# Optimization experiments

Hardware: AMD Instinct MI355X
Metric: run time of the kernel (lower is better)

## Reference

```python
import jax, jax.numpy as jnp
import numpy as np

TGT_LEN, BS, SRC_LEN, VOCAB, DIM, EMB = 24, 16, 400, 32000, 256, 256


def setup_inputs() -> dict:
    key = jax.random.key(0)
    ks = jax.random.split(key, 16)
    g = lambda k, s, sc: jax.random.normal(k, s, dtype=jnp.float32) * sc
    return {
        "inputs": jax.random.randint(ks[0], (TGT_LEN, BS), 0, VOCAB),
        "src": jax.random.randint(ks[1], (SRC_LEN, BS), 0, VOCAB),
        "h_e": g(ks[2], (SRC_LEN, BS, DIM), 0.1),
        "h0": g(ks[3], (BS, DIM), 0.1),
        "c0": g(ks[4], (BS, DIM), 0.1),
        "W_emb": g(ks[5], (VOCAB, EMB), 0.05),
        "W_ih": g(ks[6], (4 * DIM, EMB), 0.05),
        "b_ih": g(ks[7], (4 * DIM,), 0.05),
        "W_hh": g(ks[8], (4 * DIM, DIM), 0.05),
        "b_hh": g(ks[9], (4 * DIM,), 0.05),
        "W_attn_enc": g(ks[10], (DIM, DIM), 0.05),
        "W_attn_dec": g(ks[11], (DIM, DIM), 0.05),
        "W_proj": g(ks[12], (EMB, 3 * DIM), 0.05),
        "W_u": g(ks[13], (1, 3 * DIM), 0.05),
        "b_u": g(ks[14], (1,), 0.05),
        "b_out": g(ks[15], (VOCAB, 1), 0.05),
        "pad_id": 1,
    }


def reference(inputs, src, h_e, h0, c0, W_emb, W_ih, b_ih, W_hh, b_hh,
              W_attn_enc, W_attn_dec, W_proj, W_u, b_u, b_out, pad_id):
    tgt_len, bs = inputs.shape
    vocab = W_emb.shape[0]
    dim = h0.shape[1]

    emb_seq = W_emb[inputs]                       # [T, bs, emb]
    # weight-shared output projection (sect 2.4), loop-invariant -> hoisted
    W_out = jnp.tanh(W_emb @ W_proj)              # [vocab, 3*dim]
    b_out_v = b_out[:, 0]                         # [vocab]
    w_u = W_u[0]                                  # [3*dim]
    src_ids = src.T                               # [bs, src_len]
    rows = jnp.arange(bs)[:, None]
    pos = jnp.arange(tgt_len)

    def lstm_cell(x, h, c):
        gates = x @ W_ih.T + b_ih + h @ W_hh.T + b_hh
        i, f, g_, o = jnp.split(gates, 4, axis=1)
        c_new = jax.nn.sigmoid(f) * c + jax.nn.sigmoid(i) * jnp.tanh(g_)
        h_new = jax.nn.sigmoid(o) * jnp.tanh(c_new)
        return h_new, c_new

    def step(carry, xs):
        h, c, E_hist, hd_hist = carry
        emb_t, t = xs
        h, c = lstm_cell(emb_t, h, c)
        hd_t = h                                   # [bs, dim]
        # --- temporal encoder intra-attention (eq. 3-5) ---
        q = hd_t @ W_attn_enc                      # [bs, dim]
        expE = jnp.exp(jnp.einsum('bd,sbd->bs', q, h_e))  # [bs, src]
        EE = jnp.where(t == 0, expE, expE / E_hist)
        E_hist = jnp.where(t == 0, expE, E_hist + expE)
        A_e = EE / EE.sum(axis=1, keepdims=True)
        c_e = jnp.einsum('bs,sbd->bd', A_e, h_e)
        # --- decoder intra-attention over hd_history (includes current step) ---
        hd_hist = hd_hist.at[t].set(hd_t)          # [T, bs, dim]
        qd = hd_t @ W_attn_dec
        Ed = jnp.einsum('bd,tbd->bt', qd, hd_hist)
        mask = pos[None, :] <= t
        EEd = jnp.where(mask, jnp.exp(Ed), 0.0)
        A_d = EEd / EEd.sum(axis=1, keepdims=True)
        cd = jnp.einsum('bt,tbd->bd', A_d, hd_hist)
        cd_t = jnp.where(t == 0, jnp.zeros_like(cd), cd)  # t==0: cd is zeros
        # --- pointer-generator (sect 2.3) ---
        feat = jnp.concatenate([hd_t, c_e, cd_t], axis=1)   # [bs, 3*dim]
        p_switch = jax.nn.sigmoid(feat @ w_u + b_u[0])       # [bs]
        logits = feat @ W_out.T + b_out_v                     # [bs, vocab]
        logits = logits.at[:, pad_id].set(-jnp.inf)
        p_gen = jax.nn.softmax(logits, axis=1)
        copy = jnp.zeros((bs, vocab), logits.dtype).at[rows, src_ids].add(A_e)
        scores_t = (copy + p_gen) * p_switch[:, None]
        return (h, c, E_hist, hd_hist), scores_t

    hd_hist0 = jnp.zeros((tgt_len, bs, dim), h0.dtype)
    E_hist0 = jnp.ones((bs, h_e.shape[0]), h0.dtype)
    _, scores = jax.lax.scan(step, (h0, c0, E_hist0, hd_hist0), (emb_seq, pos))
    return scores  # [T, bs, vocab] mixed copy/gen distribution per step
```

## Files before the change

### kernel.cpp

```cpp
#include <hip/hip_runtime.h>
#include <cstdint>
#include <cstddef>

#define TGT   24
#define BS    16
#define SRC   400
#define VOCABN 32000
#define DIM   256
#define NROW  (TGT*BS)
#define LSTM_NBLK 4

typedef __bf16 bf16_t;
typedef __bf16 v8bf __attribute__((ext_vector_type(8)));
typedef float  v4f  __attribute__((ext_vector_type(4)));
typedef unsigned int u32;

__device__ __forceinline__ float fast_tanh(float x) {
    float e = __expf(2.f*x);
    return 1.f - 2.f/(e + 1.f);
}

__global__ void k_prep(const float* __restrict__ Whh, const float* __restrict__ Wad,
                       const float* __restrict__ he,  const float* __restrict__ Wemb,
                       const float* __restrict__ Wproj, const float* __restrict__ Wae,
                       const float* __restrict__ Wih, const int* __restrict__ inputs,
                       const float* __restrict__ h0,
                       bf16_t* o_whh, bf16_t* o_wadT, bf16_t* o_he, bf16_t* o_heT,
                       bf16_t* o_wae, bf16_t* o_wih, bf16_t* o_wprojT, bf16_t* o_embA,
                       bf16_t* o_hhi, bf16_t* o_hlo)
{
    const long S0=262144, S1=65536, S2=1638400, S3=1638400, S4=65536, S5=262144, S6=196608, S7=98304, S8=4096;
    const long total = S0+S1+S2+S3+S4+S5+S6+S7+S8;
    for (long i = (long)blockIdx.x*blockDim.x + threadIdx.x; i < total;
         i += (long)gridDim.x*blockDim.x) {
        long j = i;
        if (j < S0) { o_whh[j] = (bf16_t)Whh[j]; continue; }           j -= S0;
        if (j < S1) { long n = j>>8, k = j&255; o_wadT[j] = (bf16_t)Wad[k*DIM + n]; continue; } j -= S1;
        if (j < S2) { o_he[j] = (bf16_t)he[j]; continue; }             j -= S2;
        if (j < S3) {
            long b = j / 102400, rem = j % 102400, d = rem / 400, s = rem % 400;
            o_heT[j] = (bf16_t)he[(s*BS + b)*DIM + d]; continue; }     j -= S3;
        if (j < S4) { o_wae[j] = (bf16_t)Wae[j]; continue; }           j -= S4;
        if (j < S5) { o_wih[j] = (bf16_t)Wih[j]; continue; }           j -= S5;
        if (j < S6) { long n = j>>8, k = j&255; o_wprojT[j] = (bf16_t)Wproj[k*768 + n]; continue; } j -= S6;
        if (j < S7) { long r = j>>8, k = j&255; o_embA[j] = (bf16_t)Wemb[(long)inputs[r]*DIM + k]; continue; } j -= S7;
        {
          float v = h0[j];
          bf16_t hi = (bf16_t)v;
          o_hhi[j] = hi; o_hlo[j] = (bf16_t)(v - (float)hi); }
    }
}

__device__ __forceinline__ void gemm_tile(
    const int tid, bf16_t* As, bf16_t* Bs,
    const bf16_t* __restrict__ A, const float* __restrict__ A32,
    const bf16_t* __restrict__ B,
    const int tileIdx, const int N, const int K, const int Ntiles, const int mode,
    float* __restrict__ outF, bf16_t* __restrict__ outB,
    const float* __restrict__ bias0, const float* __restrict__ bias1)
{
    const int mt   = tileIdx / Ntiles, nt = tileIdx % Ntiles;
    const int m0   = mt*128, n0 = nt*128;
    const int lane = tid & 63, wave = tid >> 6;
    const int wm   = wave >> 1, wn = wave & 1;
    const int quad = lane >> 4, l16 = lane & 15;

    v4f acc[4][4];
#pragma unroll
    for (int i=0;i<4;i++)
#pragma unroll
        for (int j=0;j<4;j++) acc[i][j] = (v4f){0.f,0.f,0.f,0.f};

    const int srow = tid >> 1, shalf = tid & 1;
    const bf16_t* Ag   = A   ? A   + (size_t)(m0+srow)*K + shalf*16 : nullptr;
    const float*  Ag32 = A32 ? A32 + (size_t)(m0+srow)*K + shalf*16 : nullptr;
    const bf16_t* Bg = B + (size_t)(n0+srow)*K + shalf*16;
    bf16_t* AsW = &As[srow*40 + shalf*16];
    bf16_t* BsW = &Bs[srow*40 + shalf*16];

    for (int kc = 0; kc < K; kc += 32) {
        __syncthreads();
        uint4 b0 = *(const uint4*)(Bg + kc);
        uint4 b1 = *(const uint4*)(Bg + kc + 8);
        if (A32) {
            float4 f0 = *(const float4*)(Ag32 + kc);
            float4 f1 = *(const float4*)(Ag32 + kc + 4);
            float4 f2 = *(const float4*)(Ag32 + kc + 8);
            float4 f3 = *(const float4*)(Ag32 + kc + 12);
            v8bf u0, u1;
            u0[0]=(bf16_t)f0.x; u0[1]=(bf16_t)f0.y; u0[2]=(bf16_t)f0.z; u0[3]=(bf16_t)f0.w;
            u0[4]=(bf16_t)f1.x; u0[5]=(bf16_t)f1.y; u0[6]=(bf16_t)f1.z; u0[7]=(bf16_t)f1.w;
            u1[0]=(bf16_t)f2.x; u1[1]=(bf16_t)f2.y; u1[2]=(bf16_t)f2.z; u1[3]=(bf16_t)f2.w;
            u1[4]=(bf16_t)f3.x; u1[5]=(bf16_t)f3.y; u1[6]=(bf16_t)f3.z; u1[7]=(bf16_t)f3.w;
            *(v8bf*)AsW = u0; *(v8bf*)(AsW+8) = u1;
        } else {
            uint4 a0 = *(const uint4*)(Ag + kc);
            uint4 a1 = *(const uint4*)(Ag + kc + 8);
            *(uint4*)AsW = a0; *(uint4*)(AsW+8) = a1;
        }
        *(uint4*)BsW = b0; *(uint4*)(BsW+8) = b1;
        __syncthreads();
        v8bf af[4], bb[4];
#pragma unroll
        for (int i=0;i<4;i++) {
            af[i] = *(const v8bf*)&As[(wm*64 + i*16 + l16)*40 + quad*8];
            bb[i] = *(const v8bf*)&Bs[(wn*64 + i*16 + l16)*40 + quad*8];
        }
#pragma unroll
        for (int i=0;i<4;i++)
#pragma unroll
            for (int j=0;j<4;j++)
                acc[i][j] = __builtin_amdgcn_mfma_f32_16x16x32_bf16(af[i], bb[j], acc[i][j], 0,0,0);
    }

#pragma unroll
    for (int i=0;i<4;i++) {
#pragma unroll
        for (int j=0;j<4;j++) {
#pragma unroll
            for (int r=0;r<4;r++) {
                const int gr = m0 + wm*64 + i*16 + quad*4 + r;
                const int gc = n0 + wn*64 + j*16 + l16;
                const float v = acc[i][j][r];
                if (mode == 0)      outF[(size_t)gr*N + gc] = v + bias0[gc] + bias1[gc];
                else if (mode == 1) outB[(size_t)gr*N + gc] = (bf16_t)fast_tanh(v);
                else if (mode == 2) outB[(size_t)gr*N + gc] = (bf16_t)v;
                else if (mode == 4) outF[(size_t)gr*N + (gc & 255)*4 + (gc >> 8)] = v + bias0[gc] + bias1[gc];
            }
        }
    }
}

__global__ __launch_bounds__(256) void k_gemm2(
    const bf16_t* __restrict__ embA, const bf16_t* __restrict__ wih,
    float* __restrict__ xg, const float* __restrict__ b_ih, const float* __restrict__ b_hh,
    const bf16_t* __restrict__ heA, const bf16_t* __restrict__ waeB, bf16_t* __restrict__ keB)
{
    __shared__ bf16_t As[128*40];
    __shared__ bf16_t Bs[128*40];
    if (blockIdx.x < 24)
        gemm_tile(threadIdx.x, As, Bs, embA, nullptr, wih, blockIdx.x, 1024, 256, 8, 4,
                  xg, nullptr, b_ih, b_hh);
    else
        gemm_tile(threadIdx.x, As, Bs, heA, nullptr, waeB, blockIdx.x - 24, 256, 256, 2, 2,
                  nullptr, keB, nullptr, nullptr);
}

__global__ __launch_bounds__(256) void k_gemm3(
    const bf16_t* __restrict__ A, const bf16_t* __restrict__ B,
    float* __restrict__ outF, const float* __restrict__ bias0,
    const int* __restrict__ padp, float* __restrict__ rsum)
{
    __shared__ bf16_t As[128*72];
    __shared__ bf16_t Bs[128*72];
    const int tid = threadIdx.x;
    const int mt = blockIdx.x / 250, nt = blockIdx.x % 250;
    const int m0 = mt*128, n0 = nt*128;
    const int lane = tid & 63, wave = tid >> 6;
    const int wm = wave >> 1, wn = wave & 1;
    const int quad = lane >> 4, l16 = lane & 15;

    v4f acc[4][4];
#pragma unroll
    for (int i=0;i<4;i++)
#pragma unroll
        for (int j=0;j<4;j++) acc[i][j] = (v4f){0.f,0.f,0.f,0.f};

    const int srow = tid >> 1, shalf = tid & 1;
    const bf16_t* Ag = A + (size_t)(m0+srow)*768 + shalf*32;
    const bf16_t* Bg = B + (size_t)(n0+srow)*768 + shalf*32;
    bf16_t* AsW = &As[srow*72 + shalf*32];
    bf16_t* BsW = &Bs[srow*72 + shalf*32];

    for (int kc = 0; kc < 768; kc += 64) {
        __syncthreads();
        uint4 a0 = *(const uint4*)(Ag + kc);
        uint4 a1 = *(const uint4*)(Ag + kc + 8);
        uint4 a2 = *(const uint4*)(Ag + kc + 16);
        uint4 a3 = *(const uint4*)(Ag + kc + 24);
        uint4 b0 = *(const uint4*)(Bg + kc);
        uint4 b1 = *(const uint4*)(Bg + kc + 8);
        uint4 b2 = *(const uint4*)(Bg + kc + 16);
        uint4 b3 = *(const uint4*)(Bg + kc + 24);
        *(uint4*)(AsW)    = a0; *(uint4*)(AsW+8)  = a1;
        *(uint4*)(AsW+16) = a2; *(uint4*)(AsW+24) = a3;
        *(uint4*)(BsW)    = b0; *(uint4*)(BsW+8)  = b1;
        *(uint4*)(BsW+16) = b2; *(uint4*)(BsW+24) = b3;
        __syncthreads();
#pragma unroll
        for (int kk = 0; kk < 2; ++kk) {
            v8bf af[4], bb[4];
#pragma unroll
            for (int i=0;i<4;i++) {
                af[i] = *(const v8bf*)&As[(wm*64 + i*16 + l16)*72 + kk*32 + quad*8];
                bb[i] = *(const v8bf*)&Bs[(wn*64 + i*16 + l16)*72 + kk*32 + quad*8];
            }
#pragma unroll
            for (int i=0;i<4;i++)
#pragma unroll
                for (int j=0;j<4;j++)
                    acc[i][j] = __builtin_amdgcn_mfma_f32_16x16x32_bf16(af[i], bb[j], acc[i][j], 0,0,0);
        }
    }

    const int pad = *padp;
    float* rs = (float*)As;
    __syncthreads();
    if (tid < 128) rs[tid] = 0.f;
    __syncthreads();
#pragma unroll
    for (int i=0;i<4;i++) {
        float rloc[4] = {0.f,0.f,0.f,0.f};
#pragma unroll
        for (int j=0;j<4;j++) {
#pragma unroll
            for (int r=0;r<4;r++) {
                const int gr = m0 + wm*64 + i*16 + quad*4 + r;
                const int gc = n0 + wn*64 + j*16 + l16;
                const float ex = (gc == pad) ? 0.f : __expf(acc[i][j][r] + bias0[gc]);
                outF[(size_t)gr*VOCABN + gc] = ex;
                rloc[r] += ex;
            }
        }
#pragma unroll
        for (int r=0;r<4;r++)
            atomicAdd(&rs[wm*64 + i*16 + quad*4 + r], rloc[r]);
    }
    __syncthreads();
    if (tid < 128) atomicAdd(&rsum[m0 + tid], rs[tid]);
}

__device__ __forceinline__ void gridbar(int* bar, int target) {
    __syncthreads();
    if (threadIdx.x == 0) {
        __threadfence();
        __hip_atomic_fetch_add(bar, 1, __ATOMIC_ACQ_REL, __HIP_MEMORY_SCOPE_AGENT);
        while (__hip_atomic_load(bar, __ATOMIC_ACQUIRE, __HIP_MEMORY_SCOPE_AGENT) < target) { }
        __threadfence();
    }
    __syncthreads();
}

__global__ __launch_bounds__(512, 2) void k_lstm(
    const bf16_t* __restrict__ Whh, const float* __restrict__ xgT,
    const float* __restrict__ c0,
    bf16_t* __restrict__ hhiG, bf16_t* __restrict__ hloG,
    float* __restrict__ hallF, bf16_t* __restrict__ hallB,
    int* __restrict__ bar)
{
    __shared__ float gl[16][260];

    const int tid = threadIdx.x;
    const int k = blockIdx.x;
    const int w = tid >> 6, lane = tid & 63;
    const int l16 = lane & 15, quad = lane >> 4;

    v8bf wb[2][8];
#pragma unroll
    for (int ct = 0; ct < 2; ++ct) {
        const int c = w*32 + ct*16 + l16;
        const int row = (c >> 6)*256 + k*64 + (c & 63);
#pragma unroll
        for (int kc = 0; kc < 8; ++kc)
            wb[ct][kc] = *(const v8bf*)&Whh[(size_t)row*DIM + kc*32 + quad*8];
    }

    float cst[2];
#pragma unroll
    for (int e = 0; e < 2; ++e) {
        const int li = tid + e*512;
        cst[e] = c0[(li >> 6)*DIM + k*64 + (li & 63)];
    }

    for (int step = 0; step < TGT; ++step) {
        v8bf ahi[8], alo[8];
#pragma unroll
        for (int kc = 0; kc < 8; ++kc) {
            ahi[kc] = *(const v8bf*)&hhiG[l16*DIM + kc*32 + quad*8];
            alo[kc] = *(const v8bf*)&hloG[l16*DIM + kc*32 + quad*8];
        }
        float4 xv[2];
#pragma unroll
        for (int e = 0; e < 2; ++e) {
            const int li = tid + e*512;
            const int b = li >> 6, dd = li & 63;
            xv[e] = *(const float4*)&xgT[((size_t)(step*BS + b)*DIM + k*64 + dd)*4];
        }

        v4f acc[2] = {(v4f){0.f,0.f,0.f,0.f}, (v4f){0.f,0.f,0.f,0.f}};
#pragma unroll
        for (int kc = 0; kc < 8; ++kc)
#pragma unroll
            for (int ct = 0; ct < 2; ++ct) {
                acc[ct] = __builtin_amdgcn_mfma_f32_16x16x32_bf16(ahi[kc], wb[ct][kc], acc[ct], 0,0,0);
                acc[ct] = __builtin_amdgcn_mfma_f32_16x16x32_bf16(alo[kc], wb[ct][kc], acc[ct], 0,0,0);
            }
#pragma unroll
        for (int ct = 0; ct < 2; ++ct) {
            const int c = w*32 + ct*16 + l16;
#pragma unroll
            for (int r = 0; r < 4; ++r)
                gl[quad*4 + r][c] = acc[ct][r];
        }
        __syncthreads();
#pragma unroll
        for (int e = 0; e < 2; ++e) {
            const int li = tid + e*512;
            const int b = li >> 6, dd = li & 63;
            const int d = k*64 + dd;
            const float gi = gl[b][dd]        + xv[e].x;
            const float gf = gl[b][64 + dd]   + xv[e].y;
            const float gg = gl[b][128 + dd]  + xv[e].z;
            const float go = gl[b][192 + dd]  + xv[e].w;
            const float si = 1.f/(1.f+__expf(-gi));
            const float sf = 1.f/(1.f+__expf(-gf));
            const float so = 1.f/(1.f+__expf(-go));
            const float cn = sf*cst[e] + si*fast_tanh(gg);
            const float hn = so*fast_tanh(cn);
            cst[e] = cn;
            const bf16_t hi = (bf16_t)hn;
            hhiG[b*DIM + d] = hi;
            hloG[b*DIM + d] = (bf16_t)(hn - (float)hi);
            hallF[(size_t)(step*BS + b)*DIM + d] = hn;
            hallB[(size_t)(step*BS + b)*DIM + d] = hi;
        }
        if (step < TGT-1) gridbar(bar, (step+1)*LSTM_NBLK);
    }
}

__device__ __forceinline__ void escore_body(const int blk, const int tid, float* hS,
    const bf16_t* __restrict__ ke, const float* __restrict__ hallF, float* __restrict__ expE)
{
    const int t = blk >> 4, b = blk & 15;
    hS[tid] = hallF[(size_t)(t*BS + b)*DIM + tid];
    __syncthreads();
    for (int s = tid; s < SRC; s += 256) {
        const v8bf* kp = (const v8bf*)(ke + ((size_t)s*BS + b)*DIM);
        float e = 0.f;
#pragma unroll 8
        for (int m=0;m<32;m++) {
            v8bf kv = kp[m];
#pragma unroll
            for (int i=0;i<8;i++) e += (float)kv[i]*hS[m*8+i];
        }
        expE[((size_t)t*BS + b)*SRC + s] = __expf(e);
    }
}

__global__ __launch_bounds__(256) void k_esq(
    const bf16_t* __restrict__ ke, const float* __restrict__ hallF, float* __restrict__ expE,
    const bf16_t* __restrict__ hallB, const bf16_t* __restrict__ wadT, bf16_t* __restrict__ qdG)
{
    __shared__ __align__(16) char shb[20480];
    if (blockIdx.x < NROW) {
        escore_body(blockIdx.x, threadIdx.x, (float*)shb, ke, hallF, expE);
        return;
    }
    gemm_tile(threadIdx.x, (bf16_t*)shb, (bf16_t*)(shb + 10240), hallB, nullptr, wadT,
              blockIdx.x - NROW, 256, 256, 2, 2, nullptr, qdG, nullptr, nullptr);
}

__global__ __launch_bounds__(256) void k_prefix(float* __restrict__ expE)
{
    const int i = blockIdx.x*256 + threadIdx.x;
    if (i >= BS*SRC) return;
    const int b = i / SRC, s = i % SRC;
    float c = 0.f;
    for (int t = 0; t < TGT; ++t) {
        const size_t idx = ((size_t)t*BS + b)*SRC + s;
        c += expE[idx];
        expE[idx] = c;
    }
}

__device__ void attn_body(char* sh, const int blk, const int tid,
    const float* __restrict__ cumE, const bf16_t* __restrict__ heT,
    const float* __restrict__ hallF, const bf16_t* __restrict__ qdG,
    const float* __restrict__ wu, const float* __restrict__ bu,
    bf16_t* __restrict__ feat, float* __restrict__ Ae, float* __restrict__ ps)
{
    float* hS   = (float*)sh;
    float* qdS  = hS + 256;
    float* eeS  = qdS + 256;
    float* adS  = eeS + 400;
    float* red  = adS + 24;
    float* misc = red + 4;
    const int t = blk >> 4, b = blk & 15;

    hS[tid]  = hallF[(size_t)(t*BS + b)*DIM + tid];
    qdS[tid] = (float)qdG[(size_t)(t*BS + b)*DIM + tid];
    __syncthreads();

    for (int s = tid; s < SRC; s += 256) {
        if (t == 0) {
            eeS[s] = cumE[(size_t)b*SRC + s];
        } else {
            const float prev = cumE[((size_t)(t-1)*BS + b)*SRC + s];
            const float cur  = cumE[((size_t)t*BS + b)*SRC + s];
            eeS[s] = (cur - prev) / prev;
        }
    }
    __syncthreads();
    {
        float pa = 0.f;
        for (int s = tid; s < SRC; s += 256) pa += eeS[s];
#pragma unroll
        for (int o=32;o>0;o>>=1) pa += __shfl_down(pa, o);
        if ((tid & 63) == 0) red[tid>>6] = pa;
        __syncthreads();
        if (tid == 0) misc[0] = 1.f/(red[0]+red[1]+red[2]+red[3]);
        __syncthreads();
    }
    const float inv_es = misc[0];
    for (int s = tid; s < SRC; s += 256)
        Ae[((size_t)t*BS + b)*SRC + s] = eeS[s] * inv_es;

    float ce;
    {
        const v8bf* hp = (const v8bf*)(heT + ((size_t)b*DIM + tid)*SRC);
        float acc = 0.f;
#pragma unroll 10
        for (int m=0;m<50;m++) {
            v8bf hv = hp[m];
#pragma unroll
            for (int i=0;i<8;i++) acc += (float)hv[i]*eeS[m*8+i];
        }
        ce = acc * inv_es;
    }

    {
        const int wv = tid >> 6, ln = tid & 63;
        for (int tau = wv; tau <= t; tau += 4) {
            float4 a = *(const float4*)(hallF + ((size_t)(tau*BS + b))*DIM + ln*4);
            float e = a.x*qdS[ln*4] + a.y*qdS[ln*4+1] + a.z*qdS[ln*4+2] + a.w*qdS[ln*4+3];
#pragma unroll
            for (int o=32;o>0;o>>=1) e += __shfl_down(e, o);
            if (ln == 0) adS[tau] = __expf(e);
        }
    }
    __syncthreads();
    if (tid < 64) {
        float v = (tid <= t) ? adS[tid] : 0.f;
#pragma unroll
        for (int o=32;o>0;o>>=1) v += __shfl_down(v, o);
        if (tid == 0) misc[1] = 1.f/v;
    }
    __syncthreads();
    float cd = 0.f;
    for (int tau = 0; tau <= t; ++tau)
        cd += adS[tau] * hallF[((size_t)(tau*BS + b))*DIM + tid];
    cd *= misc[1];
    if (t == 0) cd = 0.f;

    const float hd = hS[tid];
    const size_t fr = ((size_t)t*BS + b)*768;
    feat[fr + tid]       = (bf16_t)hd;
    feat[fr + 256 + tid] = (bf16_t)ce;
    feat[fr + 512 + tid] = (bf16_t)cd;
    float pw = hd*wu[tid] + ce*wu[256 + tid] + cd*wu[512 + tid];
#pragma unroll
    for (int o=32;o>0;o>>=1) pw += __shfl_down(pw, o);
    if ((tid & 63) == 0) red[tid>>6] = pw;
    __syncthreads();
    if (tid == 0) {
        float s = red[0]+red[1]+red[2]+red[3];
        ps[t*BS + b] = 1.f/(1.f+__expf(-(s + bu[0])));
    }
}

__global__ __launch_bounds__(256) void k_attnw(
    const float* __restrict__ cumE, const bf16_t* __restrict__ heT,
    const float* __restrict__ hallF, const bf16_t* __restrict__ qdG,
    const float* __restrict__ wu, const float* __restrict__ bu,
    bf16_t* __restrict__ feat, float* __restrict__ Ae, float* __restrict__ ps,
    const float* __restrict__ Wemb, const bf16_t* __restrict__ wprojT,
    bf16_t* __restrict__ woutB)
{
    __shared__ __align__(16) char shb[20480];
    if (blockIdx.x < NROW) {
        attn_body(shb, blockIdx.x, threadIdx.x, cumE, heT, hallF, qdG, wu, bu, feat, Ae, ps);
        return;
    }
    gemm_tile(threadIdx.x, (bf16_t*)shb, (bf16_t*)(shb + 10240), nullptr, Wemb, wprojT,
              blockIdx.x - NROW, 768, 256, 6, 1,
              nullptr, woutB, nullptr, nullptr);
}

__global__ __launch_bounds__(256) void k_final(
    float* __restrict__ out, const float* __restrict__ rsum,
    const float* __restrict__ ps, const int* __restrict__ src,
    const float* __restrict__ Ae)
{
    const int r = blockIdx.x;
    const int b = r & (BS-1);
    const float p  = ps[r];
    const float sc = p / rsum[r];
    float4* o4 = (float4*)(out + (size_t)r*VOCABN);
    for (int i = threadIdx.x; i < VOCABN/4; i += 256) {
        float4 v = o4[i];
        v.x*=sc; v.y*=sc; v.z*=sc; v.w*=sc;
        o4[i] = v;
    }
    __syncthreads();
    for (int s = threadIdx.x; s < SRC; s += 256) {
        const int v = src[s*BS + b];
        atomicAdd(&out[(size_t)r*VOCABN + v], Ae[(size_t)r*SRC + s] * p);
    }
}

#define O_WHH    0u
#define O_WADT   524288u
#define O_HEBF   655360u
#define O_HET    3932160u
#define O_KE     7208960u
#define O_WAE    10485760u
#define O_WPROJT 10616832u
#define O_WIH    11010048u
#define O_EMBA   11534336u
#define O_WOUT   11730944u
#define O_XG     60882944u
#define O_HALLF  62455808u
#define O_HALLB  62849024u
#define O_QD     63045632u
#define O_EXPE   63242240u
#define O_FEAT   63856640u
#define O_AE     64446464u
#define O_PS     65060864u
#define O_BAR    65062400u
#define O_RSUM   65063936u

extern "C" void kernel_launch(void* const* d_in, const int* in_sizes, int n_in,
                              void* d_out, int out_size, void* d_ws, size_t ws_size,
                              hipStream_t stream)
{
    const int*   inputs = (const int*)  d_in[0];
    const int*   src    = (const int*)  d_in[1];
    const float* h_e    = (const float*)d_in[2];
    const float* h0     = (const float*)d_in[3];
    const float* c0     = (const float*)d_in[4];
    const float* W_emb  = (const float*)d_in[5];
    const float* W_ih   = (const float*)d_in[6];
    const float* b_ih   = (const float*)d_in[7];
    const float* W_hh   = (const float*)d_in[8];
    const float* b_hh   = (const float*)d_in[9];
    const float* W_ae   = (const float*)d_in[10];
    const float* W_ad   = (const float*)d_in[11];
    const float* W_proj = (const float*)d_in[12];
    const float* W_u    = (const float*)d_in[13];
    const float* b_u    = (const float*)d_in[14];
    const float* b_out  = (const float*)d_in[15];
    const int*   pad_id = (const int*)  d_in[16];

    char* w = (char*)d_ws;
    bf16_t* whh_bf  = (bf16_t*)(w + O_WHH);
    bf16_t* wadT_bf = (bf16_t*)(w + O_WADT);
    bf16_t* he_bf   = (bf16_t*)(w + O_HEBF);
    bf16_t* heT_bf  = (bf16_t*)(w + O_HET);
    bf16_t* ke_bf   = (bf16_t*)(w + O_KE);
    bf16_t* wae_bf  = (bf16_t*)(w + O_WAE);
    bf16_t* wprojT  = (bf16_t*)(w + O_WPROJT);
    bf16_t* wih_bf  = (bf16_t*)(w + O_WIH);
    bf16_t* embA_bf = (bf16_t*)(w + O_EMBA);
    bf16_t* wout_bf = (bf16_t*)(w + O_WOUT);
    float*  xg      = (float*) (w + O_XG);
    float*  hallF   = (float*) (w + O_HALLF);
    bf16_t* hallB   = (bf16_t*)(w + O_HALLB);
    bf16_t* qdG     = (bf16_t*)(w + O_QD);
    float*  expE    = (float*) (w + O_EXPE);
    bf16_t* hhiG    = (bf16_t*)(w + O_EXPE);
    bf16_t* hloG    = (bf16_t*)(w + O_EXPE + 8192);
    bf16_t* feat_bf = (bf16_t*)(w + O_FEAT);
    float*  Ae      = (float*) (w + O_AE);
    float*  ps      = (float*) (w + O_PS);
    int*    bar     = (int*)   (w + O_BAR);
    float*  rsum    = (float*) (w + O_RSUM);
    float*  out     = (float*)d_out;

    k_prep<<<1024, 256, 0, stream>>>(W_hh, W_ad, h_e, W_emb, W_proj, W_ae, W_ih, inputs, h0,
                                     whh_bf, wadT_bf, he_bf, heT_bf,
                                     wae_bf, wih_bf, wprojT, embA_bf, hhiG, hloG);
    hipMemsetAsync(w + O_BAR, 0, 3072, stream);
    k_gemm2<<<124, 256, 0, stream>>>(embA_bf, wih_bf, xg, b_ih, b_hh,
                                     he_bf, wae_bf, ke_bf);
    k_lstm<<<LSTM_NBLK, 512, 0, stream>>>(whh_bf, xg, c0, hhiG, hloG,
                                          hallF, hallB, bar);
    k_esq<<<NROW + 6, 256, 0, stream>>>(ke_bf, hallF, expE, hallB, wadT_bf, qdG);
    k_prefix<<<25, 256, 0, stream>>>(expE);
    k_attnw<<<NROW + 1500, 256, 0, stream>>>(expE, heT_bf, hallF, qdG, W_u, b_u,
                                             feat_bf, Ae, ps,
                                             W_emb, wprojT, wout_bf);
    k_gemm3<<<750, 256, 0, stream>>>(feat_bf, wout_bf, out, b_out, pad_id, rsum);
    k_final<<<NROW, 256, 0, stream>>>(out, rsum, ps, src, Ae);
}
```

Before: 436.9 us.

## Pack LSTM hidden state hi/lo into u32 and trim per-step global traffic

The LSTM recurrence now stores the bf16 hi/lo split of h as one packed 32-bit word, so each step does one load stream and one atomic store instead of two. The hallF history write is moved after the grid barrier so it stays off the serial critical path. The bf16 copy of the history (hallB) is dropped and the qd GEMM reads the fp32 history directly. The memset of the barrier region is folded into the prep kernel to save a launch. The risks are extra unpack instructions inside the recurrence and reliance on relaxed atomic stores for visibility across blocks.

Result: no change. 439.8 us (+0.7%).

```diff
diff --git a/kernel.cpp b/kernel.cpp
--- a/kernel.cpp
+++ b/kernel.cpp
@@ -14,6 +14,7 @@
 typedef __bf16 v8bf __attribute__((ext_vector_type(8)));
 typedef float  v4f  __attribute__((ext_vector_type(4)));
 typedef unsigned int u32;
+typedef unsigned short u16;
 
 __device__ __forceinline__ float fast_tanh(float x) {
     float e = __expf(2.f*x);
@@ -27,10 +28,10 @@
                        const float* __restrict__ h0,
                        bf16_t* o_whh, bf16_t* o_wadT, bf16_t* o_he, bf16_t* o_heT,
                        bf16_t* o_wae, bf16_t* o_wih, bf16_t* o_wprojT, bf16_t* o_embA,
-                       bf16_t* o_hhi, bf16_t* o_hlo)
-{
-    const long S0=262144, S1=65536, S2=1638400, S3=1638400, S4=65536, S5=262144, S6=196608, S7=98304, S8=4096;
-    const long total = S0+S1+S2+S3+S4+S5+S6+S7+S8;
+                       u32* o_hpk, u32* o_zero)
+{
+    const long S0=262144, S1=65536, S2=1638400, S3=1638400, S4=65536, S5=262144, S6=196608, S7=98304, S8=4096, S9=768;
+    const long total = S0+S1+S2+S3+S4+S5+S6+S7+S8+S9;
     for (long i = (long)blockIdx.x*blockDim.x + threadIdx.x; i < total;
          i += (long)gridDim.x*blockDim.x) {
         long j = i;
@@ -44,10 +45,13 @@
         if (j < S5) { o_wih[j] = (bf16_t)Wih[j]; continue; }           j -= S5;
         if (j < S6) { long n = j>>8, k = j&255; o_wprojT[j] = (bf16_t)Wproj[k*768 + n]; continue; } j -= S6;
         if (j < S7) { long r = j>>8, k = j&255; o_embA[j] = (bf16_t)Wemb[(long)inputs[r]*DIM + k]; continue; } j -= S7;
-        {
-          float v = h0[j];
-          bf16_t hi = (bf16_t)v;
-          o_hhi[j] = hi; o_hlo[j] = (bf16_t)(v - (float)hi); }
+        if (j < S8) {
+            float v = h0[j];
+            bf16_t hi = (bf16_t)v;
+            bf16_t lo = (bf16_t)(v - (float)hi);
+            o_hpk[j] = (u32)(*(const u16*)&hi) | ((u32)(*(const u16*)&lo) << 16);
+            continue; }                                                j -= S8;
+        o_zero[j] = 0;
     }
 }
 
@@ -244,8 +248,8 @@
 __global__ __launch_bounds__(512, 2) void k_lstm(
     const bf16_t* __restrict__ Whh, const float* __restrict__ xgT,
     const float* __restrict__ c0,
-    bf16_t* __restrict__ hhiG, bf16_t* __restrict__ hloG,
-    float* __restrict__ hallF, bf16_t* __restrict__ hallB,
+    u32* __restrict__ hpk,
+    float* __restrict__ hallF,
     int* __restrict__ bar)
 {
     __shared__ float gl[16][260];
@@ -273,11 +277,11 @@
     }
 
     for (int step = 0; step < TGT; ++step) {
-        v8bf ahi[8], alo[8];
+        uint4 pq[8][2];
 #pragma unroll
         for (int kc = 0; kc < 8; ++kc) {
-            ahi[kc] = *(const v8bf*)&hhiG[l16*DIM + kc*32 + quad*8];
-            alo[kc] = *(const v8bf*)&hloG[l16*DIM + kc*32 + quad*8];
+            const uint4* pp = (const uint4*)&hpk[l16*DIM + kc*32 + quad*8];
+            pq[kc][0] = pp[0]; pq[kc][1] = pp[1];
         }
         float4 xv[2];
 #pragma unroll
@@ -286,6 +290,18 @@
             const int b = li >> 6, dd = li & 63;
             xv[e] = *(const float4*)&xgT[((size_t)(step*BS + b)*DIM + k*64 + dd)*4];
         }
+        v8bf ahi[8], alo[8];
+#pragma unroll
+        for (int kc = 0; kc < 8; ++kc) {
+            const u32 uu[8] = {pq[kc][0].x, pq[kc][0].y, pq[kc][0].z, pq[kc][0].w,
+                               pq[kc][1].x, pq[kc][1].y, pq[kc][1].z, pq[kc][1].w};
+#pragma unroll
+            for (int j = 0; j < 8; ++j) {
+                union { u32 u; u16 s[2]; } x; x.u = uu[j];
+                ahi[kc][j] = *(const bf16_t*)&x.s[0];
+                alo[kc][j] = *(const bf16_t*)&x.s[1];
+            }
+        }
 
         v4f acc[2] = {(v4f){0.f,0.f,0.f,0.f}, (v4f){0.f,0.f,0.f,0.f}};
 #pragma unroll
@@ -303,6 +319,7 @@
                 gl[quad*4 + r][c] = acc[ct][r];
         }
         __syncthreads();
+        float hnv[2];
 #pragma unroll
         for (int e = 0; e < 2; ++e) {
             const int li = tid + e*512;
@@ -318,13 +335,22 @@
             const float cn = sf*cst[e] + si*fast_tanh(gg);
             const float hn = so*fast_tanh(cn);
             cst[e] = cn;
+            hnv[e] = hn;
             const bf16_t hi = (bf16_t)hn;
-            hhiG[b*DIM + d] = hi;
-            hloG[b*DIM + d] = (bf16_t)(hn - (float)hi);
-            hallF[(size_t)(step*BS + b)*DIM + d] = hn;
-            hallB[(size_t)(step*BS + b)*DIM + d] = hi;
+            const bf16_t lo = (bf16_t)(hn - (float)hi);
+            const u32 pk = (u32)(*(const u16*)&hi) | ((u32)(*(const u16*)&lo) << 16);
+            __hip_atomic_store(&hpk[b*DIM + d], pk, __ATOMIC_RELAXED, __HIP_MEMORY_SCOPE_AGENT);
         }
         if (step < TGT-1) gridbar(bar, (step+1)*LSTM_NBLK);
+#pragma unroll
+        for (int e = 0; e < 2; ++e) {
+            const int li = tid + e*512;
+            const int b = li >> 6, dd = li & 63;
+            const int d = k*64 + dd;
+            union { float f; u32 u; } cv; cv.f = hnv[e];
+            __hip_atomic_store((u32*)&hallF[(size_t)(step*BS + b)*DIM + d], cv.u,
+                               __ATOMIC_RELAXED, __HIP_MEMORY_SCOPE_AGENT);
+        }
     }
 }
 
@@ -349,14 +375,14 @@
 
 __global__ __launch_bounds__(256) void k_esq(
     const bf16_t* __restrict__ ke, const float* __restrict__ hallF, float* __restrict__ expE,
-    const bf16_t* __restrict__ hallB, const bf16_t* __restrict__ wadT, bf16_t* __restrict__ qdG)
+    const bf16_t* __restrict__ wadT, bf16_t* __restrict__ qdG)
 {
     __shared__ __align__(16) char shb[20480];
     if (blockIdx.x < NROW) {
         escore_body(blockIdx.x, threadIdx.x, (float*)shb, ke, hallF, expE);
         return;
     }
-    gemm_tile(threadIdx.x, (bf16_t*)shb, (bf16_t*)(shb + 10240), hallB, nullptr, wadT,
+    gemm_tile(threadIdx.x, (bf16_t*)shb, (bf16_t*)(shb + 10240), nullptr, hallF, wadT,
               blockIdx.x - NROW, 256, 256, 2, 2, nullptr, qdG, nullptr, nullptr);
 }
 
@@ -520,7 +546,6 @@
 #define O_WOUT   11730944u
 #define O_XG     60882944u
 #define O_HALLF  62455808u
-#define O_HALLB  62849024u
 #define O_QD     63045632u
 #define O_EXPE   63242240u
 #define O_FEAT   63856640u
@@ -564,27 +589,24 @@
     bf16_t* wout_bf = (bf16_t*)(w + O_WOUT);
     float*  xg      = (float*) (w + O_XG);
     float*  hallF   = (float*) (w + O_HALLF);
-    bf16_t* hallB   = (bf16_t*)(w + O_HALLB);
     bf16_t* qdG     = (bf16_t*)(w + O_QD);
     float*  expE    = (float*) (w + O_EXPE);
-    bf16_t* hhiG    = (bf16_t*)(w + O_EXPE);
-    bf16_t* hloG    = (bf16_t*)(w + O_EXPE + 8192);
+    u32*    hpk     = (u32*)   (w + O_EXPE);
     bf16_t* feat_bf = (bf16_t*)(w + O_FEAT);
     float*  Ae      = (float*) (w + O_AE);
     float*  ps      = (float*) (w + O_PS);
     int*    bar     = (int*)   (w + O_BAR);
+    u32*    zeroreg = (u32*)   (w + O_BAR);
     float*  rsum    = (float*) (w + O_RSUM);
     float*  out     = (float*)d_out;
 
     k_prep<<<1024, 256, 0, stream>>>(W_hh, W_ad, h_e, W_emb, W_proj, W_ae, W_ih, inputs, h0,
                                      whh_bf, wadT_bf, he_bf, heT_bf,
-                                     wae_bf, wih_bf, wprojT, embA_bf, hhiG, hloG);
-    hipMemsetAsync(w + O_BAR, 0, 3072, stream);
+                                     wae_bf, wih_bf, wprojT, embA_bf, hpk, zeroreg);
     k_gemm2<<<124, 256, 0, stream>>>(embA_bf, wih_bf, xg, b_ih, b_hh,
                                      he_bf, wae_bf, ke_bf);
-    k_lstm<<<LSTM_NBLK, 512, 0, stream>>>(whh_bf, xg, c0, hhiG, hloG,
-                                          hallF, hallB, bar);
-    k_esq<<<NROW + 6, 256, 0, stream>>>(ke_bf, hallF, expE, hallB, wadT_bf, qdG);
+    k_lstm<<<LSTM_NBLK, 512, 0, stream>>>(whh_bf, xg, c0, hpk, hallF, bar);
+    k_esq<<<NROW + 6, 256, 0, stream>>>(ke_bf, hallF, expE, wadT_bf, qdG);
     k_prefix<<<25, 256, 0, stream>>>(expE);
     k_attnw<<<NROW + 1500, 256, 0, stream>>>(expE, heT_bf, hallF, qdG, W_u, b_u,
                                              feat_bf, Ae, ps,
```
